# Performance work log

Measured on AMD Instinct MI355X. Metric: run time of the kernel, lower is better.

## Reference

```python
import jax, jax.numpy as jnp
import numpy as np

NP, NA = 200000, 100000        # paper / author node counts
EW, EC = 300000, 300000        # writes / cites edge counts
HID, H, D = 128, 4, 32         # hidden, heads, head dim
FIN_P, FIN_A, OUT = 256, 128, 16
SCALE = float(1.0 / np.sqrt(D))


def _seg_softmax(alpha, idx, n):
    # softmax over edges grouped by destination node (PyG softmax)
    m = jax.ops.segment_max(alpha, idx, num_segments=n)
    e = jnp.exp(alpha - m[idx])
    s = jax.ops.segment_sum(e, idx, num_segments=n)
    return e / (s[idx] + 1e-16)


def _edge_type(k_src, v_src, q_dst, src, dst, a_rel, m_rel, p_rel, n_dst):
    # per-relation transform at node level, then gather-attend-scatter
    kr = jnp.einsum('nhd,hde->nhe', k_src, a_rel)
    vr = jnp.einsum('nhd,hde->nhe', v_src, m_rel)
    alpha = jnp.sum(q_dst[dst] * kr[src], axis=-1) * p_rel * SCALE  # [E,H]
    alpha = _seg_softmax(alpha, dst, n_dst)
    return jax.ops.segment_sum(vr[src] * alpha[..., None], dst, num_segments=n_dst)


def setup_inputs() -> dict:
    key = jax.random.key(0)
    ks = iter(jax.random.split(key, 48))

    def nrm(shape, s=0.05):
        return jax.random.normal(next(ks), shape, jnp.float32) * s

    inp = dict(
        x_paper=nrm((NP, FIN_P), 1.0),
        x_author=nrm((NA, FIN_A), 1.0),
        writes_src=jax.random.randint(next(ks), (EW,), 0, NA, dtype=jnp.int32),
        writes_dst=jax.random.randint(next(ks), (EW,), 0, NP, dtype=jnp.int32),
        cites_src=jax.random.randint(next(ks), (EC,), 0, NP, dtype=jnp.int32),
        cites_dst=jax.random.randint(next(ks), (EC,), 0, NP, dtype=jnp.int32),
        lin_paper_w=nrm((FIN_P, HID)), lin_paper_b=jnp.zeros((HID,), jnp.float32),
        lin_author_w=nrm((FIN_A, HID)), lin_author_b=jnp.zeros((HID,), jnp.float32),
        lin_out_w=nrm((HID, OUT)), lin_out_b=jnp.zeros((OUT,), jnp.float32),
    )
    for t in ('paper', 'author'):
        for nm in ('k', 'q', 'v', 'a'):
            inp[f'{nm}_w_{t}'] = nrm((HID, HID))
            inp[f'{nm}_b_{t}'] = jnp.zeros((HID,), jnp.float32)
        inp[f'skip_{t}'] = jnp.ones((), jnp.float32)
    for e in ('writes', 'cites'):
        inp[f'a_rel_{e}'] = nrm((H, D, D), 0.18)
        inp[f'm_rel_{e}'] = nrm((H, D, D), 0.18)
        inp[f'p_rel_{e}'] = jnp.ones((H,), jnp.float32)
    return inp


def reference(x_paper, x_author, writes_src, writes_dst, cites_src, cites_dst,
              lin_paper_w, lin_paper_b, lin_author_w, lin_author_b,
              lin_out_w, lin_out_b,
              k_w_paper, k_b_paper, q_w_paper, q_b_paper, v_w_paper, v_b_paper,
              a_w_paper, a_b_paper, skip_paper,
              k_w_author, k_b_author, q_w_author, q_b_author, v_w_author, v_b_author,
              a_w_author, a_b_author, skip_author,
              a_rel_writes, m_rel_writes, p_rel_writes,
              a_rel_cites, m_rel_cites, p_rel_cites):
    # per-node-type input projection + relu
    hp = jax.nn.relu(x_paper @ lin_paper_w + lin_paper_b)
    ha = jax.nn.relu(x_author @ lin_author_w + lin_author_b)
    # HGTConv: per-node-type k/q/v, [N,H,D]
    k_p = (hp @ k_w_paper + k_b_paper).reshape(NP, H, D)
    q_p = (hp @ q_w_paper + q_b_paper).reshape(NP, H, D)
    v_p = (hp @ v_w_paper + v_b_paper).reshape(NP, H, D)
    k_a = (ha @ k_w_author + k_b_author).reshape(NA, H, D)
    v_a = (ha @ v_w_author + v_b_author).reshape(NA, H, D)
    # heterogeneous multi-relation attention, group='sum' over edge types
    out_p = _edge_type(k_a, v_a, q_p, writes_src, writes_dst,
                       a_rel_writes, m_rel_writes, p_rel_writes, NP)
    out_p = out_p + _edge_type(k_p, v_p, q_p, cites_src, cites_dst,
                               a_rel_cites, m_rel_cites, p_rel_cites, NP)
    # output projection + gated skip (paper type; only 'paper' feeds the head)
    op = jax.nn.gelu(out_p.reshape(NP, HID), approximate=False) @ a_w_paper + a_b_paper
    beta = jax.nn.sigmoid(skip_paper)
    hp = beta * op + (1.0 - beta) * hp
    return hp @ lin_out_w + lin_out_b  # [NP, OUT]
```

## Files before the change

kernel.cpp:

```cpp
#include <hip/hip_runtime.h>
#include <cstdint>

#define NP 200000
#define NA 100000
#define EW 300000
#define EC 300000
#define HID 128
#define FIN_P 256
#define FIN_A 128
#define NOUT 16
#define ATT_SCALE 0.17677669529663687f

#define NBP 1563
#define NBA 782

#define SCAN_N (2 * NP)
#define SCAN_BS 256
#define SCAN_ITEMS 4
#define SCAN_TILE 1024
#define SCAN_NB ((SCAN_N + SCAN_TILE - 1) / SCAN_TILE)

typedef short s8v __attribute__((ext_vector_type(8)));
typedef float f32x4 __attribute__((ext_vector_type(4)));
typedef unsigned short ushort_t;

__device__ __forceinline__ float gelu_f(float x) {
  return 0.5f * x * (1.0f + erff(x * 0.70710678118654752f));
}
__device__ __forceinline__ ushort_t f2bf(float f) {
  unsigned u = __float_as_uint(f);
  return (ushort_t)((u + 0x7FFFu + ((u >> 16) & 1u)) >> 16);
}
__device__ __forceinline__ unsigned pack2bf(float a, float b) {
  return (unsigned)f2bf(a) | ((unsigned)f2bf(b) << 16);
}
__device__ __forceinline__ unsigned cvtpk(float a, float b) {
  unsigned r;
  asm("v_cvt_pk_bf16_f32 %0, %1, %2" : "=v"(r) : "v"(a), "v"(b));
  return r;
}
__device__ __forceinline__ float bflo(unsigned u) { return __uint_as_float(u << 16); }
__device__ __forceinline__ float bfhi(unsigned u) { return __uint_as_float(u & 0xFFFF0000u); }

__device__ __forceinline__ void gl16(const void* g, void* l) {
  __builtin_amdgcn_global_load_lds(
      (const __attribute__((address_space(1))) void*)g,
      (__attribute__((address_space(3))) void*)l, 16, 0, 0);
}

__device__ __forceinline__ int s2row(int r) { return (r ^ (r >> 2)) & 3; }

__global__ void prep_all(
    const float* __restrict__ qw,  const float* __restrict__ qb,
    const float* __restrict__ kwp, const float* __restrict__ kbp, const float* __restrict__ arc,
    const float* __restrict__ vwp, const float* __restrict__ vbp, const float* __restrict__ mrc,
    const float* __restrict__ kwa, const float* __restrict__ kba, const float* __restrict__ arw,
    const float* __restrict__ vwa, const float* __restrict__ vba, const float* __restrict__ mrw,
    const float* __restrict__ lpw, const float* __restrict__ law,
    const float* __restrict__ aw, const float* __restrict__ ab,
    const float* __restrict__ skip, const float* __restrict__ W2, const float* __restrict__ b2,
    ushort_t* __restrict__ Wall, float* __restrict__ Ball,
    float* __restrict__ Wg, float* __restrict__ Wh, float* __restrict__ bo,
    int* __restrict__ cnt)
{
  const int b = blockIdx.x, tid = threadIdx.x;
  if (b == 0) {
    for (int idx = tid; idx < 16384; idx += 256) {
      int c = idx >> 7, r = idx & 127;
      Wall[idx] = f2bf(qw[r * 128 + c]);
    }
    for (int c = tid; c < 128; c += 256) Ball[c] = qb[c];
  } else if (b <= 4) {
    const float *W, *bias, *rel;
    switch (b) {
      case 1:  W = kwp; bias = kbp; rel = arc; break;
      case 2:  W = vwp; bias = vbp; rel = mrc; break;
      case 3:  W = kwa; bias = kba; rel = arw; break;
      default: W = vwa; bias = vba; rel = mrw; break;
    }
    for (int idx = tid; idx < 16384; idx += 256) {
      int c = idx >> 7, r = idx & 127, h = c >> 5, e = c & 31;
      float s = 0.f;
      #pragma unroll
      for (int d = 0; d < 32; ++d) s += W[r * 128 + h * 32 + d] * rel[h * 1024 + d * 32 + e];
      Wall[b * 16384 + idx] = f2bf(s);
    }
    for (int c = tid; c < 128; c += 256) {
      int h = c >> 5, e = c & 31;
      float s = 0.f;
      #pragma unroll
      for (int d = 0; d < 32; ++d) s += bias[h * 32 + d] * rel[h * 1024 + d * 32 + e];
      Ball[b * 128 + c] = s;
    }
  } else if (b == 5) {
    for (int idx = tid; idx < 16384; idx += 256) {
      int c = idx >> 7, r = idx & 127;
      Wall[5 * 16384 + idx] = f2bf(law[r * 128 + c]);
    }
  } else if (b == 6) {
    for (int idx = tid; idx < 32768; idx += 256) {
      int c = idx >> 8, r = idx & 255;
      Wall[6 * 16384 + idx] = f2bf(lpw[r * 128 + c]);
    }
  } else if (b == 7) {
    float beta = 1.0f / (1.0f + expf(-skip[0]));
    for (int idx = tid; idx < 128 * 16; idx += 256) {
      int r = idx >> 4, c = idx & 15;
      float s = 0.f;
      for (int k = 0; k < 128; ++k) s += aw[r * 128 + k] * W2[k * 16 + c];
      Wg[idx] = beta * s;
      Wh[idx] = (1.0f - beta) * W2[idx];
    }
    if (tid < 16) {
      float s = 0.f;
      for (int k = 0; k < 128; ++k) s += ab[k] * W2[k * 16 + tid];
      bo[tid] = beta * s + b2[tid];
    }
  } else {
    int chunk = SCAN_N / 8;
    int base = (b - 8) * chunk;
    for (int i = tid; i < chunk; i += 256) cnt[base + i] = 0;
  }
}

__global__ __launch_bounds__(256) void gemm_proj(
    const float* __restrict__ xp, const float* __restrict__ xa,
    const ushort_t* __restrict__ Wall,
    const float* __restrict__ bp, const float* __restrict__ ba,
    ushort_t* __restrict__ hpo, ushort_t* __restrict__ hao)
{
  __shared__ ushort_t As[4096];
  __shared__ ushort_t Bs[4096];
  const bool isP = blockIdx.x < NBP;
  const int bid = isP ? blockIdx.x : blockIdx.x - NBP;
  const float* A = isP ? xp : xa;
  const ushort_t* W = Wall + (isP ? 6 * 16384 : 5 * 16384);
  const float* bias = isP ? bp : ba;
  ushort_t* C = isP ? hpo : hao;
  const int M = isP ? NP : NA;
  const int KT = isP ? 256 : 128;

  const int tid  = threadIdx.x;
  const int lane = tid & 63;
  const int wv   = tid >> 6;
  const int wr   = wv >> 1, wc = wv & 1;
  const int l15  = lane & 15, kgl = lane >> 4;
  const int s2l  = (l15 ^ (l15 >> 2)) & 3;
  const int row0 = bid * 128;

  const int r0 = tid >> 2, kgp = tid & 3;
  const int sk = kgp ^ s2row(r0);
  int g0 = row0 + r0;       if (g0 > M - 1) g0 = M - 1;
  int g1 = row0 + r0 + 64;  if (g1 > M - 1) g1 = M - 1;
  const float* a0p = A + (size_t)g0 * KT + sk * 8;
  const float* a1p = A + (size_t)g1 * KT + sk * 8;
  const ushort_t* b0p = W + (size_t)r0 * KT + sk * 8;
  const ushort_t* b1p = W + (size_t)(r0 + 64) * KT + sk * 8;
  ushort_t* asd0 = &As[(size_t)tid * 8];
  ushort_t* asd1 = &As[(size_t)(tid + 256) * 8];

  f32x4 acc[4][4];
  #pragma unroll
  for (int i = 0; i < 4; ++i)
    #pragma unroll
    for (int j = 0; j < 4; ++j) acc[i][j] = (f32x4){0.f, 0.f, 0.f, 0.f};

  for (int kt = 0; kt < KT; kt += 32) {
    gl16(b0p + kt, &Bs[(size_t)tid * 8]);
    gl16(b1p + kt, &Bs[(size_t)(tid + 256) * 8]);
    float4 fa0 = *(const float4*)(a0p + kt);
    float4 fa1 = *(const float4*)(a0p + kt + 4);
    float4 fa2 = *(const float4*)(a1p + kt);
    float4 fa3 = *(const float4*)(a1p + kt + 4);
    uint4 v0, v1;
    v0.x = cvtpk(fa0.x, fa0.y); v0.y = cvtpk(fa0.z, fa0.w);
    v0.z = cvtpk(fa1.x, fa1.y); v0.w = cvtpk(fa1.z, fa1.w);
    v1.x = cvtpk(fa2.x, fa2.y); v1.y = cvtpk(fa2.z, fa2.w);
    v1.z = cvtpk(fa3.x, fa3.y); v1.w = cvtpk(fa3.z, fa3.w);
    *(uint4*)asd0 = v0;
    *(uint4*)asd1 = v1;
    __syncthreads();

    const s8v* As8 = (const s8v*)As;
    const s8v* Bs8 = (const s8v*)Bs;
    s8v af[4], bfv[4];
    #pragma unroll
    for (int i = 0; i < 4; ++i)
      af[i]  = As8[(wr * 64 + i * 16 + l15) * 4 + (kgl ^ s2l)];
    #pragma unroll
    for (int j = 0; j < 4; ++j)
      bfv[j] = Bs8[(wc * 64 + j * 16 + l15) * 4 + (kgl ^ s2l)];
    #pragma unroll
    for (int i = 0; i < 4; ++i)
      #pragma unroll
      for (int j = 0; j < 4; ++j)
        acc[i][j] = __builtin_amdgcn_mfma_f32_16x16x32_bf16(af[i], bfv[j], acc[i][j], 0, 0, 0);
    __syncthreads();
  }

  float bv[4];
  #pragma unroll
  for (int j = 0; j < 4; ++j) bv[j] = bias[wc * 64 + j * 16 + l15];
  #pragma unroll
  for (int i = 0; i < 4; ++i) {
    #pragma unroll
    for (int r = 0; r < 4; ++r) {
      int row = row0 + wr * 64 + i * 16 + kgl * 4 + r;
      if (row < M) {
        #pragma unroll
        for (int j = 0; j < 4; ++j) {
          float v = acc[i][j][r] + bv[j];
          v = fmaxf(v, 0.f);
          C[(size_t)row * 128 + wc * 64 + j * 16 + l15] = f2bf(v);
        }
      }
    }
  }
}

__global__ __launch_bounds__(256) void gemm_kv(
    const ushort_t* __restrict__ hpA, const ushort_t* __restrict__ haA,
    const ushort_t* __restrict__ Wall, const float* __restrict__ Ball,
    ushort_t* __restrict__ qkv, ushort_t* __restrict__ kvw)
{
  __shared__ ushort_t As[16384];
  __shared__ ushort_t Bs[16384];
  const bool isP = blockIdx.x < NBP;
  const int bid = isP ? blockIdx.x : blockIdx.x - NBP;
  const ushort_t* A = isP ? hpA : haA;
  const int M = isP ? NP : NA;
  const int base_set = isP ? 0 : 3;
  const int nsets = isP ? 3 : 2;

  const int tid  = threadIdx.x;
  const int lane = tid & 63;
  const int wv   = tid >> 6;
  const int wr   = wv >> 1, wc = wv & 1;
  const int l15  = lane & 15, kgl = lane >> 4;
  const int s2l  = (l15 ^ (l15 >> 2)) & 3;
  const int row0 = bid * 128;

  const int r0 = tid >> 2, kgp = tid & 3;
  const int sk = kgp ^ s2row(r0);
  int g0 = row0 + r0;       if (g0 > M - 1) g0 = M - 1;
  int g1 = row0 + r0 + 64;  if (g1 > M - 1) g1 = M - 1;
  const ushort_t* a0p = A + (size_t)g0 * 128 + sk * 8;
  const ushort_t* a1p = A + (size_t)g1 * 128 + sk * 8;

  #pragma unroll
  for (int t = 0; t < 4; ++t) {
    gl16(a0p + t * 32, &As[((size_t)t * 512 + tid) * 8]);
    gl16(a1p + t * 32, &As[((size_t)t * 512 + tid + 256) * 8]);
  }

  for (int si = 0; si < nsets; ++si) {
    const int set = base_set + si;
    const ushort_t* W = Wall + set * 16384;
    const float* bias = Ball + set * 128;
    ushort_t* C = isP ? (qkv + (size_t)set * NP * HID)
                      : (kvw + (size_t)(set - 3) * NA * HID);
    const ushort_t* b0p = W + (size_t)r0 * 128 + sk * 8;
    const ushort_t* b1p = W + (size_t)(r0 + 64) * 128 + sk * 8;
    #pragma unroll
    for (int t = 0; t < 4; ++t) {
      gl16(b0p + t * 32, &Bs[((size_t)t * 512 + tid) * 8]);
      gl16(b1p + t * 32, &Bs[((size_t)t * 512 + tid + 256) * 8]);
    }
    __syncthreads();

    f32x4 acc[4][4];
    #pragma unroll
    for (int i = 0; i < 4; ++i)
      #pragma unroll
      for (int j = 0; j < 4; ++j) acc[i][j] = (f32x4){0.f, 0.f, 0.f, 0.f};

    const s8v* As8 = (const s8v*)As;
    const s8v* Bs8 = (const s8v*)Bs;
    #pragma unroll
    for (int t = 0; t < 4; ++t) {
      s8v af[4], bfv[4];
      #pragma unroll
      for (int i = 0; i < 4; ++i)
        af[i]  = As8[t * 512 + (wr * 64 + i * 16 + l15) * 4 + (kgl ^ s2l)];
      #pragma unroll
      for (int j = 0; j < 4; ++j)
        bfv[j] = Bs8[t * 512 + (wc * 64 + j * 16 + l15) * 4 + (kgl ^ s2l)];
      #pragma unroll
      for (int i = 0; i < 4; ++i)
        #pragma unroll
        for (int j = 0; j < 4; ++j)
          acc[i][j] = __builtin_amdgcn_mfma_f32_16x16x32_bf16(af[i], bfv[j], acc[i][j], 0, 0, 0);
    }

    float bv[4];
    #pragma unroll
    for (int j = 0; j < 4; ++j) bv[j] = bias[wc * 64 + j * 16 + l15];
    #pragma unroll
    for (int i = 0; i < 4; ++i) {
      #pragma unroll
      for (int r = 0; r < 4; ++r) {
        int row = row0 + wr * 64 + i * 16 + kgl * 4 + r;
        if (row < M) {
          #pragma unroll
          for (int j = 0; j < 4; ++j) {
            C[(size_t)row * 128 + wc * 64 + j * 16 + l15] = f2bf(acc[i][j][r] + bv[j]);
          }
        }
      }
    }
    __syncthreads();
  }
}

__global__ void hist_k(const int* __restrict__ wdst, const int* __restrict__ cdst,
                       int* __restrict__ cnt)
{
  int t = blockIdx.x * blockDim.x + threadIdx.x;
  if (t < EW) atomicAdd(&cnt[wdst[t]], 1);
  if (t < EC) atomicAdd(&cnt[NP + cdst[t]], 1);
}

__global__ __launch_bounds__(SCAN_BS) void scan1(const int* __restrict__ cnt,
                                                 int* __restrict__ off,
                                                 int* __restrict__ bsum)
{
  __shared__ int sh[2][SCAN_BS];
  int tid = threadIdx.x;
  int base = blockIdx.x * SCAN_TILE + tid * SCAN_ITEMS;
  int v[SCAN_ITEMS]; int tsum = 0;
  #pragma unroll
  for (int i = 0; i < SCAN_ITEMS; ++i) {
    int idx = base + i;
    v[i] = (idx < SCAN_N) ? cnt[idx] : 0;
    tsum += v[i];
  }
  int p = 0;
  sh[0][tid] = tsum; __syncthreads();
  #pragma unroll
  for (int d = 1; d < SCAN_BS; d <<= 1) {
    int x = sh[p][tid] + ((tid >= d) ? sh[p][tid - d] : 0);
    sh[p ^ 1][tid] = x; __syncthreads(); p ^= 1;
  }
  int run = sh[p][tid] - tsum;
  #pragma unroll
  for (int i = 0; i < SCAN_ITEMS; ++i) {
    int idx = base + i;
    if (idx < SCAN_N) off[idx] = run;
    run += v[i];
  }
  if (tid == SCAN_BS - 1) bsum[blockIdx.x] = sh[p][tid];
}

__global__ __launch_bounds__(512) void scan2(int* __restrict__ bsum)
{
  __shared__ int sh[2][512];
  int tid = threadIdx.x;
  int v = (tid < SCAN_NB) ? bsum[tid] : 0;
  int p = 0;
  sh[0][tid] = v; __syncthreads();
  for (int d = 1; d < 512; d <<= 1) {
    int x = sh[p][tid] + ((tid >= d) ? sh[p][tid - d] : 0);
    sh[p ^ 1][tid] = x; __syncthreads(); p ^= 1;
  }
  if (tid < SCAN_NB) bsum[tid] = sh[p][tid] - v;
}

__global__ __launch_bounds__(SCAN_BS) void scan3(int* __restrict__ off, int* __restrict__ cur,
                                                 const int* __restrict__ bsum)
{
  int add = bsum[blockIdx.x];
  int base = blockIdx.x * SCAN_TILE + threadIdx.x;
  #pragma unroll
  for (int i = 0; i < SCAN_ITEMS; ++i) {
    int idx = base + i * SCAN_BS;
    if (idx < SCAN_N) { int t = off[idx] + add; off[idx] = t; cur[idx] = t; }
  }
  if (blockIdx.x == 0 && threadIdx.x == 0) off[SCAN_N] = EW + EC;
}

__global__ void fill_k(const int* __restrict__ wsrc, const int* __restrict__ wdst,
                       const int* __restrict__ csrc, const int* __restrict__ cdst,
                       int* __restrict__ cur, int* __restrict__ esrc)
{
  int t = blockIdx.x * blockDim.x + threadIdx.x;
  if (t < EW) { int p = atomicAdd(&cur[wdst[t]], 1); esrc[p] = wsrc[t] << 8; }
  if (t < EC) { int p = atomicAdd(&cur[NP + cdst[t]], 1); esrc[p] = csrc[t] << 8; }
}

__global__ __launch_bounds__(256) void node_attn(
    const int* __restrict__ off, const int* __restrict__ esrc,
    const ushort_t* __restrict__ q,
    const ushort_t* __restrict__ kr_w, const ushort_t* __restrict__ vr_w,
    const ushort_t* __restrict__ kr_c, const ushort_t* __restrict__ vr_c,
    const float* __restrict__ p_rel_w, const float* __restrict__ p_rel_c,
    ushort_t* __restrict__ out_p)
{
  int gid = blockIdx.x * blockDim.x + threadIdx.x;
  int node = gid >> 4;
  int l16 = gid & 15;
  int h = l16 >> 2;
  unsigned loff = (unsigned)(l16 * 16);

  int eb0 = off[node],      ee0 = off[node + 1];
  int eb1 = off[NP + node], ee1 = off[NP + node + 1];

  uint4 qv = *(const uint4*)(q + (size_t)node * HID + l16 * 8);

  int pi0 = (eb0 < ee0) ? eb0 : 0;
  int pi1 = (eb1 < ee1) ? eb1 : 0;
  unsigned pb0 = (unsigned)esrc[pi0] + loff;
  unsigned pb1 = (unsigned)esrc[pi1] + loff;
  uint4 pk[2], pv[2];
  pk[0] = *(const uint4*)((const char*)kr_w + pb0);
  pv[0] = *(const uint4*)((const char*)vr_w + pb0);
  pk[1] = *(const uint4*)((const char*)kr_c + pb1);
  pv[1] = *(const uint4*)((const char*)vr_c + pb1);

  float qf[8];
  {
    const unsigned* pq = (const unsigned*)&qv;
    #pragma unroll
    for (int w = 0; w < 4; ++w) { qf[2 * w] = bflo(pq[w]); qf[2 * w + 1] = bfhi(pq[w]); }
  }
  float prw = p_rel_w[h] * ATT_SCALE;
  float prc = p_rel_c[h] * ATT_SCALE;

  float t[8];
  #pragma unroll
  for (int i = 0; i < 8; ++i) t[i] = 0.f;

  #pragma unroll
  for (int r = 0; r < 2; ++r) {
    const char* krb = (const char*)((r == 0) ? kr_w : kr_c);
    const char* vrb = (const char*)((r == 0) ? vr_w : vr_c);
    float prr = (r == 0) ? prw : prc;
    int eb = (r == 0) ? eb0 : eb1;
    int ee = (r == 0) ? ee0 : ee1;

    float s = 0.f;
    float A[8];
    #pragma unroll
    for (int i = 0; i < 8; ++i) A[i] = 0.f;

    int e = eb;
    if (e < ee) {
      const unsigned* k8 = (const unsigned*)&pk[r];
      const unsigned* v8 = (const unsigned*)&pv[r];
      float d = 0.f;
      #pragma unroll
      for (int w = 0; w < 4; ++w) {
        d = fmaf(qf[2 * w], bflo(k8[w]), d);
        d = fmaf(qf[2 * w + 1], bfhi(k8[w]), d);
      }
      d += __shfl_xor(d, 1);
      d += __shfl_xor(d, 2);
      float p = __expf(d * prr);
      s += p;
      #pragma unroll
      for (int w = 0; w < 4; ++w) {
        A[2 * w]     = fmaf(p, bflo(v8[w]), A[2 * w]);
        A[2 * w + 1] = fmaf(p, bfhi(v8[w]), A[2 * w + 1]);
      }
      ++e;
    }
    for (; e < ee; ++e) {
      unsigned kb = (unsigned)esrc[e] + loff;
      uint4 kv = *(const uint4*)(krb + kb);
      uint4 vv = *(const uint4*)(vrb + kb);
      const unsigned* k8 = (const unsigned*)&kv;
      float d = 0.f;
      #pragma unroll
      for (int w = 0; w < 4; ++w) {
        d = fmaf(qf[2 * w], bflo(k8[w]), d);
        d = fmaf(qf[2 * w + 1], bfhi(k8[w]), d);
      }
      d += __shfl_xor(d, 1);
      d += __shfl_xor(d, 2);
      float p = __expf(d * prr);
      s += p;
      const unsigned* v8 = (const unsigned*)&vv;
      #pragma unroll
      for (int w = 0; w < 4; ++w) {
        A[2 * w]     = fmaf(p, bflo(v8[w]), A[2 * w]);
        A[2 * w + 1] = fmaf(p, bfhi(v8[w]), A[2 * w + 1]);
      }
    }
    float inv = 1.0f / (s + 1e-16f);
    #pragma unroll
    for (int i = 0; i < 8; ++i) t[i] = fmaf(A[i], inv, t[i]);
  }

  uint4 o;
  unsigned* po = (unsigned*)&o;
  #pragma unroll
  for (int w = 0; w < 4; ++w) po[w] = pack2bf(t[2 * w], t[2 * w + 1]);
  *(uint4*)(out_p + (size_t)node * HID + l16 * 8) = o;
}

__global__ __launch_bounds__(256) void epilogue_k(
    const ushort_t* __restrict__ out_p, const ushort_t* __restrict__ hp,
    const float* __restrict__ Wg, const float* __restrict__ Wh,
    const float* __restrict__ bo, float* __restrict__ out)
{
  __shared__ float Ts[64][129];
  __shared__ float Wgs[128][16];
  __shared__ float Whs[128][16];
  __shared__ float bs[16];
  int tid = threadIdx.x;
  int row0 = blockIdx.x * 64;

  #pragma unroll
  for (int i = 0; i < 2; ++i) {
    int idx = tid + i * 256;
    *(float4*)&Wgs[idx >> 2][(idx & 3) << 2] = *(const float4*)(Wg + (size_t)idx * 4);
    *(float4*)&Whs[idx >> 2][(idx & 3) << 2] = *(const float4*)(Wh + (size_t)idx * 4);
  }
  if (tid < 16) bs[tid] = bo[tid];

  #pragma unroll
  for (int i = 0; i < 4; ++i) {
    int idx = tid + i * 256;
    int r = idx >> 4, c8 = (idx & 15) << 3;
    uint4 g = *(const uint4*)(out_p + (size_t)(row0 + r) * HID + c8);
    const unsigned* pw = (const unsigned*)&g;
    #pragma unroll
    for (int w = 0; w < 4; ++w) {
      Ts[r][c8 + 2 * w]     = gelu_f(bflo(pw[w]));
      Ts[r][c8 + 2 * w + 1] = gelu_f(bfhi(pw[w]));
    }
  }
  __syncthreads();

  int row = tid & 63, cg = tid >> 6;
  float acc[4];
  #pragma unroll
  for (int j = 0; j < 4; ++j) acc[j] = bs[cg * 4 + j];
  for (int k = 0; k < 128; ++k) {
    float g = Ts[row][k];
    float4 w = *(const float4*)&Wgs[k][cg << 2];
    acc[0] = fmaf(g, w.x, acc[0]); acc[1] = fmaf(g, w.y, acc[1]);
    acc[2] = fmaf(g, w.z, acc[2]); acc[3] = fmaf(g, w.w, acc[3]);
  }
  __syncthreads();

  #pragma unroll
  for (int i = 0; i < 4; ++i) {
    int idx = tid + i * 256;
    int r = idx >> 4, c8 = (idx & 15) << 3;
    uint4 hh = *(const uint4*)(hp + (size_t)(row0 + r) * HID + c8);
    const unsigned* pw = (const unsigned*)&hh;
    #pragma unroll
    for (int w = 0; w < 4; ++w) {
      Ts[r][c8 + 2 * w]     = bflo(pw[w]);
      Ts[r][c8 + 2 * w + 1] = bfhi(pw[w]);
    }
  }
  __syncthreads();
  for (int k = 0; k < 128; ++k) {
    float hv = Ts[row][k];
    float4 w = *(const float4*)&Whs[k][cg << 2];
    acc[0] = fmaf(hv, w.x, acc[0]); acc[1] = fmaf(hv, w.y, acc[1]);
    acc[2] = fmaf(hv, w.z, acc[2]); acc[3] = fmaf(hv, w.w, acc[3]);
  }
  *(float4*)(out + (size_t)(row0 + row) * NOUT + (cg << 2)) =
      make_float4(acc[0], acc[1], acc[2], acc[3]);
}

extern "C" void kernel_launch(void* const* d_in, const int* in_sizes, int n_in,
                              void* d_out, int out_size, void* d_ws, size_t ws_size,
                              hipStream_t stream)
{
  (void)in_sizes; (void)n_in; (void)out_size; (void)ws_size;
  const float* x_paper      = (const float*)d_in[0];
  const float* x_author     = (const float*)d_in[1];
  const int*   writes_src   = (const int*)d_in[2];
  const int*   writes_dst   = (const int*)d_in[3];
  const int*   cites_src    = (const int*)d_in[4];
  const int*   cites_dst    = (const int*)d_in[5];
  const float* lin_paper_w  = (const float*)d_in[6];
  const float* lin_paper_b  = (const float*)d_in[7];
  const float* lin_author_w = (const float*)d_in[8];
  const float* lin_author_b = (const float*)d_in[9];
  const float* lin_out_w    = (const float*)d_in[10];
  const float* lin_out_b    = (const float*)d_in[11];
  const float* k_w_paper    = (const float*)d_in[12];
  const float* k_b_paper    = (const float*)d_in[13];
  const float* q_w_paper    = (const float*)d_in[14];
  const float* q_b_paper    = (const float*)d_in[15];
  const float* v_w_paper    = (const float*)d_in[16];
  const float* v_b_paper    = (const float*)d_in[17];
  const float* a_w_paper    = (const float*)d_in[18];
  const float* a_b_paper    = (const float*)d_in[19];
  const float* skip_paper   = (const float*)d_in[20];
  const float* k_w_author   = (const float*)d_in[21];
  const float* k_b_author   = (const float*)d_in[22];
  const float* v_w_author   = (const float*)d_in[25];
  const float* v_b_author   = (const float*)d_in[26];
  const float* a_rel_writes = (const float*)d_in[30];
  const float* m_rel_writes = (const float*)d_in[31];
  const float* p_rel_writes = (const float*)d_in[32];
  const float* a_rel_cites  = (const float*)d_in[33];
  const float* m_rel_cites  = (const float*)d_in[34];
  const float* p_rel_cites  = (const float*)d_in[35];

  float* ws = (float*)d_ws;
  size_t off_f = 0;
  auto nxt = [&](size_t nfloats) { float* p = ws + off_f; off_f += nfloats; return p; };
  ushort_t* hp    = (ushort_t*)nxt((size_t)NP * 64);
  ushort_t* ha    = (ushort_t*)nxt((size_t)NA * 64);
  ushort_t* qkv   = (ushort_t*)nxt((size_t)3 * NP * 64);
  ushort_t* kvw   = (ushort_t*)nxt((size_t)2 * NA * 64);
  ushort_t* outp  = (ushort_t*)nxt((size_t)NP * 64);
  int*      cnt   = (int*)nxt(SCAN_N);
  int*      offs  = (int*)nxt(SCAN_N + 2);
  int*      cur   = (int*)nxt(SCAN_N);
  int*      esrc  = (int*)nxt(EW + EC);
  int*      bsum  = (int*)nxt(512);
  ushort_t* Wall  = (ushort_t*)nxt(65536);
  float*    Ball  = nxt(5 * 128);
  float*    Wg    = nxt(2048);
  float*    Wh    = nxt(2048);
  float*    bo    = nxt(16);

  ushort_t* q_p  = qkv;
  ushort_t* kr_c = qkv + (size_t)NP * HID;
  ushort_t* vr_c = qkv + (size_t)2 * NP * HID;
  ushort_t* kr_w = kvw;
  ushort_t* vr_w = kvw + (size_t)NA * HID;

  prep_all<<<16, 256, 0, stream>>>(q_w_paper, q_b_paper,
                                   k_w_paper, k_b_paper, a_rel_cites,
                                   v_w_paper, v_b_paper, m_rel_cites,
                                   k_w_author, k_b_author, a_rel_writes,
                                   v_w_author, v_b_author, m_rel_writes,
                                   lin_paper_w, lin_author_w,
                                   a_w_paper, a_b_paper, skip_paper, lin_out_w, lin_out_b,
                                   Wall, Ball, Wg, Wh, bo, cnt);

  hist_k<<<(300000 + 255) / 256, 256, 0, stream>>>(writes_dst, cites_dst, cnt);
  scan1<<<SCAN_NB, SCAN_BS, 0, stream>>>(cnt, offs, bsum);
  scan2<<<1, 512, 0, stream>>>(bsum);
  scan3<<<SCAN_NB, SCAN_BS, 0, stream>>>(offs, cur, bsum);
  fill_k<<<(300000 + 255) / 256, 256, 0, stream>>>(writes_src, writes_dst,
                                                   cites_src, cites_dst, cur, esrc);

  gemm_proj<<<NBP + NBA, 256, 0, stream>>>(x_paper, x_author, Wall,
                                           lin_paper_b, lin_author_b, hp, ha);
  gemm_kv<<<NBP + NBA, 256, 0, stream>>>(hp, ha, Wall, Ball, qkv, kvw);

  node_attn<<<(NP * 16) / 256, 256, 0, stream>>>(
      offs, esrc, q_p, kr_w, vr_w, kr_c, vr_c, p_rel_writes, p_rel_cites, outp);

  epilogue_k<<<(NP + 63) / 64, 256, 0, stream>>>(outp, hp, Wg, Wh, bo, (float*)d_out);
}
```

Measured before the change: 425.3 us.

## Double-buffer LDS tiles in projection GEMM to overlap loads with MFMA

Converts the input projection GEMM's single-buffered shared-memory tiles into a ping-pong double buffer. The next K-slice's global loads and bf16 conversion now overlap with the MFMA work on the current slice, and one of the two barriers per iteration goes away. It also adds launch_bounds(256,1), which doubles LDS use and may lower occupancy, reducing the latency hiding that multiple resident blocks would otherwise give.

```diff
diff --git a/kernel.cpp b/kernel.cpp
--- a/kernel.cpp
+++ b/kernel.cpp
@@ -123,14 +123,14 @@
   }
 }
 
-__global__ __launch_bounds__(256) void gemm_proj(
+__global__ __launch_bounds__(256, 1) void gemm_proj(
     const float* __restrict__ xp, const float* __restrict__ xa,
     const ushort_t* __restrict__ Wall,
     const float* __restrict__ bp, const float* __restrict__ ba,
     ushort_t* __restrict__ hpo, ushort_t* __restrict__ hao)
 {
-  __shared__ ushort_t As[4096];
-  __shared__ ushort_t Bs[4096];
+  __shared__ ushort_t As[2][4096];
+  __shared__ ushort_t Bs[2][4096];
   const bool isP = blockIdx.x < NBP;
   const int bid = isP ? blockIdx.x : blockIdx.x - NBP;
   const float* A = isP ? xp : xa;
@@ -139,6 +139,7 @@
   ushort_t* C = isP ? hpo : hao;
   const int M = isP ? NP : NA;
   const int KT = isP ? 256 : 128;
+  const int nt = KT >> 5;
 
   const int tid  = threadIdx.x;
   const int lane = tid & 63;
@@ -156,8 +157,6 @@
   const float* a1p = A + (size_t)g1 * KT + sk * 8;
   const ushort_t* b0p = W + (size_t)r0 * KT + sk * 8;
   const ushort_t* b1p = W + (size_t)(r0 + 64) * KT + sk * 8;
-  ushort_t* asd0 = &As[(size_t)tid * 8];
-  ushort_t* asd1 = &As[(size_t)(tid + 256) * 8];
 
   f32x4 acc[4][4];
   #pragma unroll
@@ -165,24 +164,39 @@
     #pragma unroll
     for (int j = 0; j < 4; ++j) acc[i][j] = (f32x4){0.f, 0.f, 0.f, 0.f};
 
-  for (int kt = 0; kt < KT; kt += 32) {
-    gl16(b0p + kt, &Bs[(size_t)tid * 8]);
-    gl16(b1p + kt, &Bs[(size_t)(tid + 256) * 8]);
-    float4 fa0 = *(const float4*)(a0p + kt);
-    float4 fa1 = *(const float4*)(a0p + kt + 4);
-    float4 fa2 = *(const float4*)(a1p + kt);
-    float4 fa3 = *(const float4*)(a1p + kt + 4);
+  {
+    gl16(b0p, &Bs[0][(size_t)tid * 8]);
+    gl16(b1p, &Bs[0][(size_t)(tid + 256) * 8]);
+    float4 fa0 = *(const float4*)(a0p);
+    float4 fa1 = *(const float4*)(a0p + 4);
+    float4 fa2 = *(const float4*)(a1p);
+    float4 fa3 = *(const float4*)(a1p + 4);
     uint4 v0, v1;
     v0.x = cvtpk(fa0.x, fa0.y); v0.y = cvtpk(fa0.z, fa0.w);
     v0.z = cvtpk(fa1.x, fa1.y); v0.w = cvtpk(fa1.z, fa1.w);
     v1.x = cvtpk(fa2.x, fa2.y); v1.y = cvtpk(fa2.z, fa2.w);
     v1.z = cvtpk(fa3.x, fa3.y); v1.w = cvtpk(fa3.z, fa3.w);
-    *(uint4*)asd0 = v0;
-    *(uint4*)asd1 = v1;
-    __syncthreads();
-
-    const s8v* As8 = (const s8v*)As;
-    const s8v* Bs8 = (const s8v*)Bs;
+    *(uint4*)&As[0][(size_t)tid * 8] = v0;
+    *(uint4*)&As[0][(size_t)(tid + 256) * 8] = v1;
+  }
+  __syncthreads();
+
+  int cur = 0;
+  for (int t = 0; t < nt; ++t) {
+    const bool more = (t + 1) < nt;
+    const int ktn = (t + 1) * 32;
+    float4 fa0, fa1, fa2, fa3;
+    if (more) {
+      gl16(b0p + ktn, &Bs[cur ^ 1][(size_t)tid * 8]);
+      gl16(b1p + ktn, &Bs[cur ^ 1][(size_t)(tid + 256) * 8]);
+      fa0 = *(const float4*)(a0p + ktn);
+      fa1 = *(const float4*)(a0p + ktn + 4);
+      fa2 = *(const float4*)(a1p + ktn);
+      fa3 = *(const float4*)(a1p + ktn + 4);
+    }
+
+    const s8v* As8 = (const s8v*)&As[cur][0];
+    const s8v* Bs8 = (const s8v*)&Bs[cur][0];
     s8v af[4], bfv[4];
     #pragma unroll
     for (int i = 0; i < 4; ++i)
@@ -195,7 +209,18 @@
       #pragma unroll
       for (int j = 0; j < 4; ++j)
         acc[i][j] = __builtin_amdgcn_mfma_f32_16x16x32_bf16(af[i], bfv[j], acc[i][j], 0, 0, 0);
+
+    if (more) {
+      uint4 v0, v1;
+      v0.x = cvtpk(fa0.x, fa0.y); v0.y = cvtpk(fa0.z, fa0.w);
+      v0.z = cvtpk(fa1.x, fa1.y); v0.w = cvtpk(fa1.z, fa1.w);
+      v1.x = cvtpk(fa2.x, fa2.y); v1.y = cvtpk(fa2.z, fa2.w);
+      v1.z = cvtpk(fa3.x, fa3.y); v1.w = cvtpk(fa3.z, fa3.w);
+      *(uint4*)&As[cur ^ 1][(size_t)tid * 8] = v0;
+      *(uint4*)&As[cur ^ 1][(size_t)(tid + 256) * 8] = v1;
+    }
     __syncthreads();
+    cur ^= 1;
   }
 
   float bv[4];
```

After: 426.2 us. Within noise of the previous version (+0.2%).

## Move output epilogue to bf16 MFMA and widen input-projection K tile

Applied to the files above, without the earlier changes.

The scalar FP32 epilogue, which ran two 128x16 dot products per row from LDS, is replaced by an MFMA kernel. It multiplies the concatenation [gelu(out_p), hp] by a prepacked bf16 256x16 weight that folds in beta and the output projection. gemm_proj now stages 64 K values per barrier instead of 32, halving the sync count, and is marked launch_bounds(256,1). The epilogue weights and GELU outputs are now rounded to bf16, which adds precision loss, and the occupancy hint may reduce latency hiding in gemm_proj.

```diff
diff --git a/kernel.cpp b/kernel.cpp
--- a/kernel.cpp
+++ b/kernel.cpp
@@ -60,7 +60,7 @@
     const float* __restrict__ aw, const float* __restrict__ ab,
     const float* __restrict__ skip, const float* __restrict__ W2, const float* __restrict__ b2,
     ushort_t* __restrict__ Wall, float* __restrict__ Ball,
-    float* __restrict__ Wg, float* __restrict__ Wh, float* __restrict__ bo,
+    ushort_t* __restrict__ Wcatb, float* __restrict__ bo,
     int* __restrict__ cnt)
 {
   const int b = blockIdx.x, tid = threadIdx.x;
@@ -104,12 +104,17 @@
     }
   } else if (b == 7) {
     float beta = 1.0f / (1.0f + expf(-skip[0]));
-    for (int idx = tid; idx < 128 * 16; idx += 256) {
-      int r = idx >> 4, c = idx & 15;
-      float s = 0.f;
-      for (int k = 0; k < 128; ++k) s += aw[r * 128 + k] * W2[k * 16 + c];
-      Wg[idx] = beta * s;
-      Wh[idx] = (1.0f - beta) * W2[idx];
+    for (int idx = tid; idx < 4096; idx += 256) {
+      int c = idx >> 8, k = idx & 255;
+      float v;
+      if (k < 128) {
+        float s = 0.f;
+        for (int j = 0; j < 128; ++j) s += aw[k * 128 + j] * W2[j * 16 + c];
+        v = beta * s;
+      } else {
+        v = (1.0f - beta) * W2[(k - 128) * 16 + c];
+      }
+      Wcatb[c * 256 + k] = f2bf(v);
     }
     if (tid < 16) {
       float s = 0.f;
@@ -123,14 +128,14 @@
   }
 }
 
-__global__ __launch_bounds__(256) void gemm_proj(
+__global__ __launch_bounds__(256, 1) void gemm_proj(
     const float* __restrict__ xp, const float* __restrict__ xa,
     const ushort_t* __restrict__ Wall,
     const float* __restrict__ bp, const float* __restrict__ ba,
     ushort_t* __restrict__ hpo, ushort_t* __restrict__ hao)
 {
-  __shared__ ushort_t As[4096];
-  __shared__ ushort_t Bs[4096];
+  __shared__ ushort_t As[8192];
+  __shared__ ushort_t Bs[8192];
   const bool isP = blockIdx.x < NBP;
   const int bid = isP ? blockIdx.x : blockIdx.x - NBP;
   const float* A = isP ? xp : xa;
@@ -139,6 +144,7 @@
   ushort_t* C = isP ? hpo : hao;
   const int M = isP ? NP : NA;
   const int KT = isP ? 256 : 128;
+  const int nt = KT >> 6;
 
   const int tid  = threadIdx.x;
   const int lane = tid & 63;
@@ -156,8 +162,6 @@
   const float* a1p = A + (size_t)g1 * KT + sk * 8;
   const ushort_t* b0p = W + (size_t)r0 * KT + sk * 8;
   const ushort_t* b1p = W + (size_t)(r0 + 64) * KT + sk * 8;
-  ushort_t* asd0 = &As[(size_t)tid * 8];
-  ushort_t* asd1 = &As[(size_t)(tid + 256) * 8];
 
   f32x4 acc[4][4];
   #pragma unroll
@@ -165,36 +169,52 @@
     #pragma unroll
     for (int j = 0; j < 4; ++j) acc[i][j] = (f32x4){0.f, 0.f, 0.f, 0.f};
 
-  for (int kt = 0; kt < KT; kt += 32) {
-    gl16(b0p + kt, &Bs[(size_t)tid * 8]);
-    gl16(b1p + kt, &Bs[(size_t)(tid + 256) * 8]);
+  for (int t = 0; t < nt; ++t) {
+    const int kt = t * 64;
+    gl16(b0p + kt,      &Bs[(size_t)tid * 8]);
+    gl16(b1p + kt,      &Bs[(size_t)(tid + 256) * 8]);
+    gl16(b0p + kt + 32, &Bs[(size_t)(tid + 512) * 8]);
+    gl16(b1p + kt + 32, &Bs[(size_t)(tid + 768) * 8]);
     float4 fa0 = *(const float4*)(a0p + kt);
     float4 fa1 = *(const float4*)(a0p + kt + 4);
     float4 fa2 = *(const float4*)(a1p + kt);
     float4 fa3 = *(const float4*)(a1p + kt + 4);
-    uint4 v0, v1;
-    v0.x = cvtpk(fa0.x, fa0.y); v0.y = cvtpk(fa0.z, fa0.w);
-    v0.z = cvtpk(fa1.x, fa1.y); v0.w = cvtpk(fa1.z, fa1.w);
-    v1.x = cvtpk(fa2.x, fa2.y); v1.y = cvtpk(fa2.z, fa2.w);
-    v1.z = cvtpk(fa3.x, fa3.y); v1.w = cvtpk(fa3.z, fa3.w);
-    *(uint4*)asd0 = v0;
-    *(uint4*)asd1 = v1;
+    float4 fb0 = *(const float4*)(a0p + kt + 32);
+    float4 fb1 = *(const float4*)(a0p + kt + 36);
+    float4 fb2 = *(const float4*)(a1p + kt + 32);
+    float4 fb3 = *(const float4*)(a1p + kt + 36);
+    uint4 v;
+    v.x = cvtpk(fa0.x, fa0.y); v.y = cvtpk(fa0.z, fa0.w);
+    v.z = cvtpk(fa1.x, fa1.y); v.w = cvtpk(fa1.z, fa1.w);
+    *(uint4*)&As[(size_t)tid * 8] = v;
+    v.x = cvtpk(fa2.x, fa2.y); v.y = cvtpk(fa2.z, fa2.w);
+    v.z = cvtpk(fa3.x, fa3.y); v.w = cvtpk(fa3.z, fa3.w);
+    *(uint4*)&As[(size_t)(tid + 256) * 8] = v;
+    v.x = cvtpk(fb0.x, fb0.y); v.y = cvtpk(fb0.z, fb0.w);
+    v.z = cvtpk(fb1.x, fb1.y); v.w = cvtpk(fb1.z, fb1.w);
+    *(uint4*)&As[(size_t)(tid + 512) * 8] = v;
+    v.x = cvtpk(fb2.x, fb2.y); v.y = cvtpk(fb2.z, fb2.w);
+    v.z = cvtpk(fb3.x, fb3.y); v.w = cvtpk(fb3.z, fb3.w);
+    *(uint4*)&As[(size_t)(tid + 768) * 8] = v;
     __syncthreads();
 
     const s8v* As8 = (const s8v*)As;
     const s8v* Bs8 = (const s8v*)Bs;
-    s8v af[4], bfv[4];
-    #pragma unroll
-    for (int i = 0; i < 4; ++i)
-      af[i]  = As8[(wr * 64 + i * 16 + l15) * 4 + (kgl ^ s2l)];
-    #pragma unroll
-    for (int j = 0; j < 4; ++j)
-      bfv[j] = Bs8[(wc * 64 + j * 16 + l15) * 4 + (kgl ^ s2l)];
-    #pragma unroll
-    for (int i = 0; i < 4; ++i)
+    #pragma unroll
+    for (int pg = 0; pg < 2; ++pg) {
+      s8v af[4], bfv[4];
+      #pragma unroll
+      for (int i = 0; i < 4; ++i)
+        af[i]  = As8[pg * 512 + (wr * 64 + i * 16 + l15) * 4 + (kgl ^ s2l)];
       #pragma unroll
       for (int j = 0; j < 4; ++j)
-        acc[i][j] = __builtin_amdgcn_mfma_f32_16x16x32_bf16(af[i], bfv[j], acc[i][j], 0, 0, 0);
+        bfv[j] = Bs8[pg * 512 + (wc * 64 + j * 16 + l15) * 4 + (kgl ^ s2l)];
+      #pragma unroll
+      for (int i = 0; i < 4; ++i)
+        #pragma unroll
+        for (int j = 0; j < 4; ++j)
+          acc[i][j] = __builtin_amdgcn_mfma_f32_16x16x32_bf16(af[i], bfv[j], acc[i][j], 0, 0, 0);
+    }
     __syncthreads();
   }
 
@@ -209,9 +229,9 @@
       if (row < M) {
         #pragma unroll
         for (int j = 0; j < 4; ++j) {
-          float v = acc[i][j][r] + bv[j];
-          v = fmaxf(v, 0.f);
-          C[(size_t)row * 128 + wc * 64 + j * 16 + l15] = f2bf(v);
+          float vv = acc[i][j][r] + bv[j];
+          vv = fmaxf(vv, 0.f);
+          C[(size_t)row * 128 + wc * 64 + j * 16 + l15] = f2bf(vv);
         }
       }
     }
@@ -497,73 +517,72 @@
   *(uint4*)(out_p + (size_t)node * HID + l16 * 8) = o;
 }
 
-__global__ __launch_bounds__(256) void epilogue_k(
+__global__ __launch_bounds__(256) void epilogue_mfma(
     const ushort_t* __restrict__ out_p, const ushort_t* __restrict__ hp,
-    const float* __restrict__ Wg, const float* __restrict__ Wh,
-    const float* __restrict__ bo, float* __restrict__ out)
-{
-  __shared__ float Ts[64][129];
-  __shared__ float Wgs[128][16];
-  __shared__ float Whs[128][16];
-  __shared__ float bs[16];
-  int tid = threadIdx.x;
-  int row0 = blockIdx.x * 64;
+    const ushort_t* __restrict__ Wcatb, const float* __restrict__ bo,
+    float* __restrict__ out)
+{
+  __shared__ ushort_t As[4096];
+  const int tid  = threadIdx.x;
+  const int lane = tid & 63;
+  const int wv   = tid >> 6;
+  const int l15  = lane & 15, kgl = lane >> 4;
+  const int s2l  = (l15 ^ (l15 >> 2)) & 3;
+  const int row0 = blockIdx.x * 128;
+
+  const int r0 = tid >> 2, kgp = tid & 3;
+  const int sk = kgp ^ s2row(r0);
+  int g0 = row0 + r0;       if (g0 > NP - 1) g0 = NP - 1;
+  int g1 = row0 + r0 + 64;  if (g1 > NP - 1) g1 = NP - 1;
+
+  s8v bfr[8];
+  #pragma unroll
+  for (int ks = 0; ks < 8; ++ks)
+    bfr[ks] = *(const s8v*)(Wcatb + (size_t)l15 * 256 + ks * 32 + kgl * 8);
+  float bo_l = bo[l15];
+
+  f32x4 acc[2];
+  acc[0] = (f32x4){0.f, 0.f, 0.f, 0.f};
+  acc[1] = (f32x4){0.f, 0.f, 0.f, 0.f};
+
+  #pragma unroll
+  for (int ph = 0; ph < 8; ++ph) {
+    if (ph < 4) {
+      const int kt = ph * 32;
+      uint4 v0 = *(const uint4*)(out_p + (size_t)g0 * 128 + kt + sk * 8);
+      uint4 v1 = *(const uint4*)(out_p + (size_t)g1 * 128 + kt + sk * 8);
+      unsigned* p0 = (unsigned*)&v0;
+      unsigned* p1 = (unsigned*)&v1;
+      #pragma unroll
+      for (int w = 0; w < 4; ++w) {
+        p0[w] = cvtpk(gelu_f(bflo(p0[w])), gelu_f(bfhi(p0[w])));
+        p1[w] = cvtpk(gelu_f(bflo(p1[w])), gelu_f(bfhi(p1[w])));
+      }
+      *(uint4*)&As[(size_t)tid * 8] = v0;
+      *(uint4*)&As[(size_t)(tid + 256) * 8] = v1;
+    } else {
+      const int kt = (ph - 4) * 32;
+      gl16(hp + (size_t)g0 * 128 + kt + sk * 8, &As[(size_t)tid * 8]);
+      gl16(hp + (size_t)g1 * 128 + kt + sk * 8, &As[(size_t)(tid + 256) * 8]);
+    }
+    __syncthreads();
+
+    const s8v* As8 = (const s8v*)As;
+    s8v af0 = As8[(wv * 32 + l15) * 4 + (kgl ^ s2l)];
+    s8v af1 = As8[(wv * 32 + 16 + l15) * 4 + (kgl ^ s2l)];
+    acc[0] = __builtin_amdgcn_mfma_f32_16x16x32_bf16(af0, bfr[ph], acc[0], 0, 0, 0);
+    acc[1] = __builtin_amdgcn_mfma_f32_16x16x32_bf16(af1, bfr[ph], acc[1], 0, 0, 0);
+    __syncthreads();
+  }
 
   #pragma unroll
   for (int i = 0; i < 2; ++i) {
-    int idx = tid + i * 256;
-    *(float4*)&Wgs[idx >> 2][(idx & 3) << 2] = *(const float4*)(Wg + (size_t)idx * 4);
-    *(float4*)&Whs[idx >> 2][(idx & 3) << 2] = *(const float4*)(Wh + (size_t)idx * 4);
-  }
-  if (tid < 16) bs[tid] = bo[tid];
-
-  #pragma unroll
-  for (int i = 0; i < 4; ++i) {
-    int idx = tid + i * 256;
-    int r = idx >> 4, c8 = (idx & 15) << 3;
-    uint4 g = *(const uint4*)(out_p + (size_t)(row0 + r) * HID + c8);
-    const unsigned* pw = (const unsigned*)&g;
-    #pragma unroll
-    for (int w = 0; w < 4; ++w) {
-      Ts[r][c8 + 2 * w]     = gelu_f(bflo(pw[w]));
-      Ts[r][c8 + 2 * w + 1] = gelu_f(bfhi(pw[w]));
-    }
-  }
-  __syncthreads();
-
-  int row = tid & 63, cg = tid >> 6;
-  float acc[4];
-  #pragma unroll
-  for (int j = 0; j < 4; ++j) acc[j] = bs[cg * 4 + j];
-  for (int k = 0; k < 128; ++k) {
-    float g = Ts[row][k];
-    float4 w = *(const float4*)&Wgs[k][cg << 2];
-    acc[0] = fmaf(g, w.x, acc[0]); acc[1] = fmaf(g, w.y, acc[1]);
-    acc[2] = fmaf(g, w.z, acc[2]); acc[3] = fmaf(g, w.w, acc[3]);
-  }
-  __syncthreads();
-
-  #pragma unroll
-  for (int i = 0; i < 4; ++i) {
-    int idx = tid + i * 256;
-    int r = idx >> 4, c8 = (idx & 15) << 3;
-    uint4 hh = *(const uint4*)(hp + (size_t)(row0 + r) * HID + c8);
-    const unsigned* pw = (const unsigned*)&hh;
-    #pragma unroll
-    for (int w = 0; w < 4; ++w) {
-      Ts[r][c8 + 2 * w]     = bflo(pw[w]);
-      Ts[r][c8 + 2 * w + 1] = bfhi(pw[w]);
-    }
-  }
-  __syncthreads();
-  for (int k = 0; k < 128; ++k) {
-    float hv = Ts[row][k];
-    float4 w = *(const float4*)&Whs[k][cg << 2];
-    acc[0] = fmaf(hv, w.x, acc[0]); acc[1] = fmaf(hv, w.y, acc[1]);
-    acc[2] = fmaf(hv, w.z, acc[2]); acc[3] = fmaf(hv, w.w, acc[3]);
-  }
-  *(float4*)(out + (size_t)(row0 + row) * NOUT + (cg << 2)) =
-      make_float4(acc[0], acc[1], acc[2], acc[3]);
+    #pragma unroll
+    for (int r = 0; r < 4; ++r) {
+      int row = row0 + wv * 32 + i * 16 + kgl * 4 + r;
+      if (row < NP) out[(size_t)row * NOUT + l15] = acc[i][r] + bo_l;
+    }
+  }
 }
 
 extern "C" void kernel_launch(void* const* d_in, const int* in_sizes, int n_in,
@@ -618,8 +637,7 @@
   int*      bsum  = (int*)nxt(512);
   ushort_t* Wall  = (ushort_t*)nxt(65536);
   float*    Ball  = nxt(5 * 128);
-  float*    Wg    = nxt(2048);
-  float*    Wh    = nxt(2048);
+  ushort_t* Wcatb = (ushort_t*)nxt(2048);
   float*    bo    = nxt(16);
 
   ushort_t* q_p  = qkv;
@@ -635,7 +653,7 @@
                                    v_w_author, v_b_author, m_rel_writes,
                                    lin_paper_w, lin_author_w,
                                    a_w_paper, a_b_paper, skip_paper, lin_out_w, lin_out_b,
-                                   Wall, Ball, Wg, Wh, bo, cnt);
+                                   Wall, Ball, Wcatb, bo, cnt);
 
   hist_k<<<(300000 + 255) / 256, 256, 0, stream>>>(writes_dst, cites_dst, cnt);
   scan1<<<SCAN_NB, SCAN_BS, 0, stream>>>(cnt, offs, bsum);
@@ -651,5 +669,5 @@
   node_attn<<<(NP * 16) / 256, 256, 0, stream>>>(
       offs, esrc, q_p, kr_w, vr_w, kr_c, vr_c, p_rel_writes, p_rel_cites, outp);
 
-  epilogue_k<<<(NP + 63) / 64, 256, 0, stream>>>(outp, hp, Wg, Wh, bo, (float*)d_out);
-}
+  epilogue_mfma<<<NBP, 256, 0, stream>>>(outp, hp, Wcatb, bo, (float*)d_out);
+}
```

Result: faster. 386.0 us (-9.2%).
